# Kernel tuning notes

Measured on AMD Instinct MI355X. Metric: run time of the kernel, lower is better.

## Reference

```python
import jax, jax.numpy as jnp
import numpy as np
from jax import lax

BIT_SIZE = 8
ES_SIZE = 1


def posit_quantize(x, nbits=BIT_SIZE, es=ES_SIZE):
    """Round x to the nearest posit(nbits, es) representable value (round-to-nearest
    of the fraction given the regime/exponent-dependent fraction width)."""
    sign = jnp.sign(x)
    a = jnp.abs(x)
    safe = jnp.where(a > 0, a, jnp.ones_like(a))
    logx = jnp.floor(jnp.log2(safe))            # binade exponent
    ipow = 2 ** es                               # 2^es, python int
    k = jnp.floor(logx / ipow)                   # regime value
    regime_len = jnp.where(k >= 0, k + 2, -k + 1)
    fbits = jnp.clip(nbits - 1 - regime_len - es, 0, 23)  # fraction bits left
    scale = jnp.exp2(logx)
    frac = safe / scale                          # in [1, 2)
    step = jnp.exp2(fbits)
    q = jnp.round(frac * step) / step * scale
    maxpos = jnp.float32(2.0 ** ((nbits - 2) * ipow))
    minpos = jnp.float32(2.0 ** (-(nbits - 2) * ipow))
    q = jnp.clip(q, minpos, maxpos)
    return jnp.where(a > 0, sign * q, jnp.zeros_like(x))


def pq(x):
    # straight-through quantizer (forward value is exact posit rounding)
    return x + lax.stop_gradient(posit_quantize(x) - x)


def conv2d(x, w):  # NCHW, OIHW, valid, stride 1
    return lax.conv_general_dilated(x, w, (1, 1), 'VALID',
                                    dimension_numbers=('NCHW', 'OIHW', 'NCHW'))


def maxpool2(x):
    return lax.reduce_window(x, -jnp.inf, lax.max,
                             (1, 1, 2, 2), (1, 1, 2, 2), 'VALID')


def setup_inputs() -> dict:
    key = jax.random.key(0)
    ks = jax.random.split(key, 9)
    B = 4096
    x = jax.random.normal(ks[0], (B, 1, 28, 28), jnp.float32)
    def init_w(k, shape, fan_in):
        bound = 1.0 / np.sqrt(fan_in)
        return jax.random.uniform(k, shape, jnp.float32, -bound, bound)
    conv1_w = init_w(ks[1], (32, 1, 3, 3), 1 * 9)
    conv1_b = init_w(ks[2], (32,), 1 * 9)
    conv2_w = init_w(ks[3], (64, 32, 3, 3), 32 * 9)
    conv2_b = init_w(ks[4], (64,), 32 * 9)
    fc1_w = init_w(ks[5], (128, 12 * 12 * 64), 12 * 12 * 64)
    fc1_b = init_w(ks[6], (128,), 12 * 12 * 64)
    fc2_w = init_w(ks[7], (10, 128), 128)
    fc2_b = init_w(ks[8], (10,), 128)
    return dict(x=x, conv1_w=conv1_w, conv1_b=conv1_b, conv2_w=conv2_w,
                conv2_b=conv2_b, fc1_w=fc1_w, fc1_b=fc1_b,
                fc2_w=fc2_w, fc2_b=fc2_b)


def reference(x, conv1_w, conv1_b, conv2_w, conv2_b, fc1_w, fc1_b, fc2_w, fc2_b):
    # PositizedConv2d: posit-quantize activations and weights, conv in fp32, add bias
    h = conv2d(pq(x), pq(conv1_w)) + conv1_b[None, :, None, None]   # [B,32,26,26]
    h = jax.nn.relu(h)
    h = conv2d(pq(h), pq(conv2_w)) + conv2_b[None, :, None, None]   # [B,64,24,24]
    h = jax.nn.relu(h)
    h = maxpool2(h)                                                  # [B,64,12,12]
    # dropout layers are identity in eval mode
    h = h.reshape(-1, 12 * 12 * 64)
    h = jax.nn.relu(jnp.dot(pq(h), pq(fc1_w).T) + fc1_b)             # [B,128]
    out = jnp.dot(pq(h), pq(fc2_w).T) + fc2_b                        # [B,10]
    return out
```

## Files before the change

kernel.cpp:

```cpp
#include <hip/hip_runtime.h>

using u16 = unsigned short;
using u32 = unsigned int;
typedef __attribute__((ext_vector_type(8))) short bf16x8;
typedef __attribute__((ext_vector_type(4))) float f32x4;

__device__ __forceinline__ float posit_q(float x) {
    float a = __builtin_fabsf(x);
    u32 u = __float_as_uint(a);
    int logx = (int)(u >> 23) - 127;
    logx = logx < -60 ? -60 : (logx > 60 ? 60 : logx);
    float frac = __uint_as_float((u & 0x007fffffu) | 0x3f800000u);
    int k = logx >> 1;
    int rl = (k >= 0) ? (k + 2) : (1 - k);
    int fb = 6 - rl; fb = fb < 0 ? 0 : fb;
    float step = (float)(1 << fb);
    float q = rintf(frac * step) * __uint_as_float((u32)(127 + logx - fb) << 23);
    q = fminf(fmaxf(q, 0x1p-12f), 0x1p12f);
    return (a > 0.0f) ? copysignf(q, x) : 0.0f;
}

__device__ __forceinline__ float b2f(u16 v) { return __uint_as_float((u32)v << 16); }
__device__ __forceinline__ u16 f2b(float f) { return (u16)(__float_as_uint(f) >> 16); }

__device__ __forceinline__ void lut_init(int tid, float* lut) {
    if (tid < 256) {
        int e = tid - 127;
        float m = 0.f;
        if (e >= -12 && e <= 12) {
            int k = e >> 1;
            int rl = max(k + 2, 1 - k);
            int fb = max(6 - rl, 0);
            m = __uint_as_float((u32)(150 + e - fb) << 23) * 1.5f;
        }
        lut[tid] = m;
    }
}
__device__ __forceinline__ u32 pq_pos_raw(float x, const float* __restrict__ lut) {
    u32 u = __float_as_uint(x);
    float c = lut[u >> 23];
    float q = (x + c) - c;
    q = fminf(fmaxf(q, 0x1p-12f), 0x1p12f);
    return u == 0u ? 0u : __float_as_uint(q);
}

__global__ __launch_bounds__(256) void prep_kernel(
    const float* __restrict__ w1, const float* __restrict__ w2,
    const float* __restrict__ fw2,
    float* __restrict__ w1q, u16* __restrict__ w2frag, float* __restrict__ fc2wq) {
    int i = blockIdx.x * 256 + threadIdx.x;
    if (i < 288)  w1q[i]   = posit_q(w1[i]);
    if (i < 1280) fc2wq[i] = posit_q(fw2[i]);
    if (i < 18432) {
        int e = i & 7, lane = (i >> 3) & 63, c9 = i >> 9;
        int kc = c9 % 9, nt = c9 / 9;
        int n = nt * 16 + (lane & 15);
        int ci = ((lane >> 4) << 3) + e;
        w2frag[i] = f2b(posit_q(w2[n * 288 + ci * 9 + kc]));
    }
}

__global__ __launch_bounds__(256) void prep2_kernel(
    const float* __restrict__ fw1, u16* __restrict__ fc1wqF) {
    int i = blockIdx.x * 256 + threadIdx.x;
    int e = i & 7, lane = (i >> 3) & 63, c = i >> 9;
    int kk = c % 288, nt = c / 288;
    int n = nt * 16 + (lane & 15);
    int k = kk * 32 + ((lane >> 4) << 3) + e;
    fc1wqF[i] = f2b(posit_q(fw1[(size_t)n * 9216 + k]));
}

#define PLS 5416
__global__ __launch_bounds__(512, 4) void conv_fused_kernel(
    const float* __restrict__ x, const float* __restrict__ w1q, const float* __restrict__ b1,
    const u16* __restrict__ w2frag, const float* __restrict__ b2,
    const float* __restrict__ fw1, u16* __restrict__ fc1wq, u16* __restrict__ pooled) {
    __shared__ __align__(16) float sX[784];
    __shared__ __align__(16) u16 sH1[4 * PLS];
    __shared__ __align__(16) u16 sPool[64 * 152];
    __shared__ float sLut[256];
    int img = blockIdx.x, tid = threadIdx.x;
    int wave = tid >> 6, lane = tid & 63;
    int col = lane & 15, quad = lane >> 4;

    lut_init(tid, sLut);

    for (int i = tid; i < 784; i += 512) sX[i] = posit_q(x[(size_t)img * 784 + i]);
    if (tid < 288) fc1wq[(size_t)img * 288 + tid] = f2b(posit_q(fw1[(size_t)img * 288 + tid]));

    int ocp = tid & 15;
    float wreg[18];
#pragma unroll
    for (int j = 0; j < 18; ++j) wreg[j] = w1q[ocp * 18 + j];
    float bias0 = b1[ocp * 2], bias1 = b1[ocp * 2 + 1];

    __syncthreads();

    int pgrp = tid >> 4;
    u16* h1dst = &sH1[(ocp >> 2) * PLS + 2 * (ocp & 3)];
    for (int it = 0; it < 22; ++it) {
        int p = it * 32 + pgrp;
        if (p < 676) {
            int y = p / 26, xx = p - y * 26;
            const float* px = &sX[y * 28 + xx];
            float in9[9];
#pragma unroll
            for (int r = 0; r < 3; ++r)
#pragma unroll
                for (int c = 0; c < 3; ++c) in9[r * 3 + c] = px[r * 28 + c];
            float a0 = bias0, a1 = bias1;
#pragma unroll
            for (int j = 0; j < 9; ++j) {
                a0 = fmaf(wreg[j], in9[j], a0);
                a1 = fmaf(wreg[9 + j], in9[j], a1);
            }
            u32 r0 = pq_pos_raw(fmaxf(a0, 0.f), sLut);
            u32 r1 = pq_pos_raw(fmaxf(a1, 0.f), sLut);
            *(u32*)&h1dst[p * 8] = (r0 >> 16) | (r1 & 0xFFFF0000u);
        }
    }

    __syncthreads();
    int npair = wave & 1, mq = wave >> 1;
    bf16x8 bfrag[2][9];
#pragma unroll
    for (int j = 0; j < 2; ++j)
#pragma unroll
        for (int kc = 0; kc < 9; ++kc)
            bfrag[j][kc] = *(const bf16x8*)(w2frag + (((npair * 2 + j) * 9 + kc) * 64 + lane) * 8);
    float cb0 = b2[(npair * 2) * 16 + col];
    float cb1 = b2[(npair * 2 + 1) * 16 + col];
    int poolb0 = ((npair * 2) * 16 + col) * 152;
    int poolb1 = ((npair * 2 + 1) * 16 + col) * 152;
    const u16* aplane = &sH1[quad * PLS];

    for (int t = 0; t < 9; ++t) {
        int mt = mq * 9 + t;
        int m = mt * 16 + col;
        int pp = m >> 2, wi = m & 3;
        int py = pp / 12, px_ = pp - py * 12;
        int oh = 2 * py + (wi >> 1), ow = 2 * px_ + (wi & 1);
        const u16* ap = aplane + (oh * 26 + ow) * 8;
        f32x4 acc0 = {0.f, 0.f, 0.f, 0.f}, acc1 = {0.f, 0.f, 0.f, 0.f};
#pragma unroll
        for (int kc = 0; kc < 9; ++kc) {
            int kh = kc / 3, kw = kc - kh * 3;
            bf16x8 af = *(const bf16x8*)(ap + (kh * 26 + kw) * 8);
            acc0 = __builtin_amdgcn_mfma_f32_16x16x32_bf16(af, bfrag[0][kc], acc0, 0, 0, 0);
            acc1 = __builtin_amdgcn_mfma_f32_16x16x32_bf16(af, bfrag[1][kc], acc1, 0, 0, 0);
        }
        float mx0 = fmaxf(fmaxf(acc0[0], acc0[1]), fmaxf(acc0[2], acc0[3]));
        float mx1 = fmaxf(fmaxf(acc1[0], acc1[1]), fmaxf(acc1[2], acc1[3]));
        sPool[poolb0 + mt * 4 + quad] = (u16)(pq_pos_raw(fmaxf(mx0 + cb0, 0.f), sLut) >> 16);
        sPool[poolb1 + mt * 4 + quad] = (u16)(pq_pos_raw(fmaxf(mx1 + cb1, 0.f), sLut) >> 16);
    }
    __syncthreads();

    for (int u = tid; u < 1152; u += 512) {
        int c = u / 18, g = u - c * 18;
        uint4 v = *(const uint4*)&sPool[c * 152 + g * 8];
        *(uint4*)(pooled + (size_t)img * 9216 + c * 144 + g * 8) = v;
    }
}

#define AS 2328
__global__ __launch_bounds__(512, 4) void fc1_part_kernel(const u16* __restrict__ pooled,
    const u16* __restrict__ fc1wqF, float* __restrict__ part) {
    __shared__ __align__(16) char smem[16 * AS * 2];
    u16* sA = (u16*)smem;
    float* sAcc = (float*)smem;
    int blk = blockIdx.x, tid = threadIdx.x;
    int mb = blk >> 2, ks = blk & 3;
    int wave = tid >> 6, lane = tid & 63;
    int row = lane & 15, quad = lane >> 4;

    {
        const u16* src = pooled + (size_t)mb * 16 * 9216 + ks * 2304;
        for (int i = tid; i < 4608; i += 512) {
            int r = i / 288, o = i - r * 288;
            *(uint4*)&sA[r * AS + o * 8] = *(const uint4*)(src + (size_t)r * 9216 + o * 8);
        }
    }
    __syncthreads();

    const bf16x8* bbase = (const bf16x8*)fc1wqF + (size_t)(ks * 72 + wave * 9) * 64 + lane;
    const u16* abase = &sA[row * AS + wave * 288 + quad * 8];
    f32x4 acc[8];
#pragma unroll
    for (int nt = 0; nt < 8; ++nt) acc[nt] = f32x4{0.f, 0.f, 0.f, 0.f};
#pragma unroll 1
    for (int k2 = 0; k2 < 9; ++k2) {
        bf16x8 a = *(const bf16x8*)(abase + k2 * 32);
        bf16x8 b[8];
#pragma unroll
        for (int nt = 0; nt < 8; ++nt)
            b[nt] = bbase[((size_t)nt * 288 + k2) * 64];
#pragma unroll
        for (int nt = 0; nt < 8; ++nt)
            acc[nt] = __builtin_amdgcn_mfma_f32_16x16x32_bf16(a, b[nt], acc[nt], 0, 0, 0);
    }
    __syncthreads();
    if (wave < 4) {
#pragma unroll
        for (int nt = 0; nt < 8; ++nt)
#pragma unroll
            for (int r = 0; r < 4; ++r)
                sAcc[wave * 2112 + (quad * 4 + r) * 132 + nt * 16 + row] = acc[nt][r];
    }
    __syncthreads();
    if (wave >= 4) {
#pragma unroll
        for (int nt = 0; nt < 8; ++nt)
#pragma unroll
            for (int r = 0; r < 4; ++r)
                sAcc[(wave - 4) * 2112 + (quad * 4 + r) * 132 + nt * 16 + row] += acc[nt][r];
    }
    __syncthreads();
    for (int e = tid; e < 2048; e += 512) {
        int o = (e >> 7) * 132 + (e & 127);
        part[(size_t)blk * 2048 + e] = sAcc[o] + sAcc[2112 + o] + sAcc[4224 + o] + sAcc[6336 + o];
    }
}

__global__ __launch_bounds__(256) void fc2_red_kernel(const float* __restrict__ part,
    const float* __restrict__ fc1b, const float* __restrict__ fc2wq,
    const float* __restrict__ fc2b, float* __restrict__ out) {
    __shared__ __align__(16) u16 sFc1[2048];
    __shared__ float sW2[1280];
    __shared__ float sB2[16];
    __shared__ float sLut[256];
    int mb = blockIdx.x, tid = threadIdx.x;
    lut_init(tid, sLut);
    for (int i = tid; i < 1280; i += 256) sW2[i] = fc2wq[i];
    if (tid < 10) sB2[tid] = fc2b[tid];
    __syncthreads();
    const float* pb = part + (size_t)mb * 4 * 2048;
    for (int e = tid; e < 2048; e += 256) {
        float s = pb[e] + pb[2048 + e] + pb[4096 + e] + pb[6144 + e];
        sFc1[e] = (u16)(pq_pos_raw(fmaxf(s + fc1b[e & 127], 0.f), sLut) >> 16);
    }
    __syncthreads();
    if (tid < 160) {
        int il = tid / 10, oc = tid - il * 10;
        float s = sB2[oc];
        const u16* hp = &sFc1[il * 128];
        const float* wp = &sW2[oc * 128];
#pragma unroll
        for (int k = 0; k < 128; ++k) s = fmaf(b2f(hp[k]), wp[k], s);
        out[(size_t)(mb * 16 + il) * 10 + oc] = s;
    }
}

extern "C" void kernel_launch(void* const* d_in, const int* in_sizes, int n_in,
                              void* d_out, int out_size, void* d_ws, size_t ws_size,
                              hipStream_t stream) {
    const float* x    = (const float*)d_in[0];
    const float* w1   = (const float*)d_in[1];
    const float* b1   = (const float*)d_in[2];
    const float* w2   = (const float*)d_in[3];
    const float* b2   = (const float*)d_in[4];
    const float* fw1  = (const float*)d_in[5];
    const float* fb1  = (const float*)d_in[6];
    const float* fw2  = (const float*)d_in[7];
    const float* fb2  = (const float*)d_in[8];
    float* out = (float*)d_out;

    char* ws = (char*)d_ws;
    float* w1q     = (float*)(ws + 0);
    float* fc2wq   = (float*)(ws + 1280);
    u16*   w2frag  = (u16*)(ws + 6400);
    u16*   fc1wqF  = (u16*)(ws + 43520);
    u16*   fc1dmy  = (u16*)(ws + 2402816);
    u16*   pooled  = (u16*)(ws + 4762112);
    float* part    = (float*)(ws + 80259584);

    prep_kernel<<<72, 256, 0, stream>>>(w1, w2, fw2, w1q, w2frag, fc2wq);
    prep2_kernel<<<4608, 256, 0, stream>>>(fw1, fc1wqF);
    conv_fused_kernel<<<4096, 512, 0, stream>>>(x, w1q, b1, w2frag, b2, fw1, fc1dmy, pooled);
    fc1_part_kernel<<<1024, 512, 0, stream>>>(pooled, fc1wqF, part);
    fc2_red_kernel<<<256, 256, 0, stream>>>(part, fb1, fc2wq, fb2, out);
}
```

Measured before the change: 249.6 us.

## Restructure conv2 MFMA loop: one N-tile per wave, 18 M-tile accumulators

Each wave now owns a single 16-column output-channel tile and half of the M tiles, keeping 18 accumulators live across a kc-outer loop. Instead of preloading 18 B fragments into registers, it loads one B fragment per kc and reuses it across the 18 M tiles. This lowers register pressure from the B fragments and raises the number of independent MFMAs in flight, but each A fragment from LDS is now read once per N tile rather than shared across two, which adds LDS traffic. The 72 accumulator VGPRs may also affect occupancy.

```diff
diff --git a/kernel.cpp b/kernel.cpp
--- a/kernel.cpp
+++ b/kernel.cpp
@@ -121,38 +121,40 @@
     }
 
     __syncthreads();
-    int npair = wave & 1, mq = wave >> 1;
-    bf16x8 bfrag[2][9];
-#pragma unroll
-    for (int j = 0; j < 2; ++j)
-#pragma unroll
-        for (int kc = 0; kc < 9; ++kc)
-            bfrag[j][kc] = *(const bf16x8*)(w2frag + (((npair * 2 + j) * 9 + kc) * 64 + lane) * 8);
-    float cb0 = b2[(npair * 2) * 16 + col];
-    float cb1 = b2[(npair * 2 + 1) * 16 + col];
-    int poolb0 = ((npair * 2) * 16 + col) * 152;
-    int poolb1 = ((npair * 2 + 1) * 16 + col) * 152;
+    int nt = wave & 3, mhalf = wave >> 2;
+    float cb = b2[nt * 16 + col];
+    int poolb = (nt * 16 + col) * 152;
     const u16* aplane = &sH1[quad * PLS];
 
-    for (int t = 0; t < 9; ++t) {
-        int mt = mq * 9 + t;
+    int aoff[18];
+#pragma unroll
+    for (int t = 0; t < 18; ++t) {
+        int mt = mhalf * 18 + t;
         int m = mt * 16 + col;
         int pp = m >> 2, wi = m & 3;
         int py = pp / 12, px_ = pp - py * 12;
         int oh = 2 * py + (wi >> 1), ow = 2 * px_ + (wi & 1);
-        const u16* ap = aplane + (oh * 26 + ow) * 8;
-        f32x4 acc0 = {0.f, 0.f, 0.f, 0.f}, acc1 = {0.f, 0.f, 0.f, 0.f};
-#pragma unroll
-        for (int kc = 0; kc < 9; ++kc) {
-            int kh = kc / 3, kw = kc - kh * 3;
-            bf16x8 af = *(const bf16x8*)(ap + (kh * 26 + kw) * 8);
-            acc0 = __builtin_amdgcn_mfma_f32_16x16x32_bf16(af, bfrag[0][kc], acc0, 0, 0, 0);
-            acc1 = __builtin_amdgcn_mfma_f32_16x16x32_bf16(af, bfrag[1][kc], acc1, 0, 0, 0);
-        }
-        float mx0 = fmaxf(fmaxf(acc0[0], acc0[1]), fmaxf(acc0[2], acc0[3]));
-        float mx1 = fmaxf(fmaxf(acc1[0], acc1[1]), fmaxf(acc1[2], acc1[3]));
-        sPool[poolb0 + mt * 4 + quad] = (u16)(pq_pos_raw(fmaxf(mx0 + cb0, 0.f), sLut) >> 16);
-        sPool[poolb1 + mt * 4 + quad] = (u16)(pq_pos_raw(fmaxf(mx1 + cb1, 0.f), sLut) >> 16);
+        aoff[t] = (oh * 26 + ow) * 8;
+    }
+    f32x4 acc[18];
+#pragma unroll
+    for (int t = 0; t < 18; ++t) acc[t] = f32x4{0.f, 0.f, 0.f, 0.f};
+#pragma unroll 1
+    for (int kc = 0; kc < 9; ++kc) {
+        int kh = kc / 3, kw = kc - kh * 3;
+        bf16x8 bfr = *(const bf16x8*)(w2frag + ((nt * 9 + kc) * 64 + lane) * 8);
+        int delta = (kh * 26 + kw) * 8;
+#pragma unroll
+        for (int t = 0; t < 18; ++t) {
+            bf16x8 af = *(const bf16x8*)(aplane + aoff[t] + delta);
+            acc[t] = __builtin_amdgcn_mfma_f32_16x16x32_bf16(af, bfr, acc[t], 0, 0, 0);
+        }
+    }
+#pragma unroll
+    for (int t = 0; t < 18; ++t) {
+        int mt = mhalf * 18 + t;
+        float mx = fmaxf(fmaxf(acc[t][0], acc[t][1]), fmaxf(acc[t][2], acc[t][3]));
+        sPool[poolb + mt * 4 + quad] = (u16)(pq_pos_raw(fmaxf(mx + cb, 0.f), sLut) >> 16);
     }
     __syncthreads();
 
```

After: 293.0 us. 17.4% more time.

## Merge prep kernels and fuse fc2 reduction into fc1 via last-block election

Applied to the files above, without the earlier changes.

The two weight-prep kernels become one launch that also zeroes a per-row-block counter array. The separate fc2 reduction kernel is folded into fc1_part_kernel: each block atomically bumps its row block's counter, and the fourth (last) block to arrive sums the partials and computes fc2 in place. This removes two kernel launches and the gaps between them, at the cost of atomics, thread fences and a serialized tail in the electing block.

```diff
diff --git a/kernel.cpp b/kernel.cpp
--- a/kernel.cpp
+++ b/kernel.cpp
@@ -44,30 +44,32 @@
     return u == 0u ? 0u : __float_as_uint(q);
 }
 
-__global__ __launch_bounds__(256) void prep_kernel(
+__global__ __launch_bounds__(256) void prep_all_kernel(
     const float* __restrict__ w1, const float* __restrict__ w2,
-    const float* __restrict__ fw2,
-    float* __restrict__ w1q, u16* __restrict__ w2frag, float* __restrict__ fc2wq) {
-    int i = blockIdx.x * 256 + threadIdx.x;
-    if (i < 288)  w1q[i]   = posit_q(w1[i]);
-    if (i < 1280) fc2wq[i] = posit_q(fw2[i]);
-    if (i < 18432) {
-        int e = i & 7, lane = (i >> 3) & 63, c9 = i >> 9;
-        int kc = c9 % 9, nt = c9 / 9;
+    const float* __restrict__ fw2, const float* __restrict__ fw1,
+    float* __restrict__ w1q, u16* __restrict__ w2frag, float* __restrict__ fc2wq,
+    u16* __restrict__ fc1wqF, int* __restrict__ cnt) {
+    int b = blockIdx.x;
+    if (b < 4608) {
+        int i = b * 256 + threadIdx.x;
+        int e = i & 7, lane = (i >> 3) & 63, c = i >> 9;
+        int kk = c % 288, nt = c / 288;
         int n = nt * 16 + (lane & 15);
-        int ci = ((lane >> 4) << 3) + e;
-        w2frag[i] = f2b(posit_q(w2[n * 288 + ci * 9 + kc]));
-    }
-}
-
-__global__ __launch_bounds__(256) void prep2_kernel(
-    const float* __restrict__ fw1, u16* __restrict__ fc1wqF) {
-    int i = blockIdx.x * 256 + threadIdx.x;
-    int e = i & 7, lane = (i >> 3) & 63, c = i >> 9;
-    int kk = c % 288, nt = c / 288;
-    int n = nt * 16 + (lane & 15);
-    int k = kk * 32 + ((lane >> 4) << 3) + e;
-    fc1wqF[i] = f2b(posit_q(fw1[(size_t)n * 9216 + k]));
+        int k = kk * 32 + ((lane >> 4) << 3) + e;
+        fc1wqF[i] = f2b(posit_q(fw1[(size_t)n * 9216 + k]));
+    } else {
+        int i = (b - 4608) * 256 + threadIdx.x;
+        if (i < 256)  cnt[i] = 0;
+        if (i < 288)  w1q[i]   = posit_q(w1[i]);
+        if (i < 1280) fc2wq[i] = posit_q(fw2[i]);
+        {
+            int e = i & 7, lane = (i >> 3) & 63, c9 = i >> 9;
+            int kc = c9 % 9, nt = c9 / 9;
+            int n = nt * 16 + (lane & 15);
+            int ci = ((lane >> 4) << 3) + e;
+            w2frag[i] = f2b(posit_q(w2[n * 288 + ci * 9 + kc]));
+        }
+    }
 }
 
 #define PLS 5416
@@ -165,8 +167,11 @@
 
 #define AS 2328
 __global__ __launch_bounds__(512, 4) void fc1_part_kernel(const u16* __restrict__ pooled,
-    const u16* __restrict__ fc1wqF, float* __restrict__ part) {
+    const u16* __restrict__ fc1wqF, float* __restrict__ part, int* __restrict__ cnt,
+    const float* __restrict__ fc1b, const float* __restrict__ fc2wq,
+    const float* __restrict__ fc2b, float* __restrict__ out) {
     __shared__ __align__(16) char smem[16 * AS * 2];
+    __shared__ int sElect;
     u16* sA = (u16*)smem;
     float* sAcc = (float*)smem;
     int blk = blockIdx.x, tid = threadIdx.x;
@@ -220,24 +225,24 @@
         int o = (e >> 7) * 132 + (e & 127);
         part[(size_t)blk * 2048 + e] = sAcc[o] + sAcc[2112 + o] + sAcc[4224 + o] + sAcc[6336 + o];
     }
-}
-
-__global__ __launch_bounds__(256) void fc2_red_kernel(const float* __restrict__ part,
-    const float* __restrict__ fc1b, const float* __restrict__ fc2wq,
-    const float* __restrict__ fc2b, float* __restrict__ out) {
-    __shared__ __align__(16) u16 sFc1[2048];
-    __shared__ float sW2[1280];
-    __shared__ float sB2[16];
-    __shared__ float sLut[256];
-    int mb = blockIdx.x, tid = threadIdx.x;
-    lut_init(tid, sLut);
-    for (int i = tid; i < 1280; i += 256) sW2[i] = fc2wq[i];
+
+    __threadfence();
+    if (tid == 0) sElect = (atomicAdd(&cnt[mb], 1) == 3);
+    __syncthreads();
+    if (!sElect) return;
+    __threadfence();
+    u16*   sFc1  = (u16*)smem;
+    float* sW2   = (float*)(smem + 4096);
+    float* sB2   = (float*)(smem + 9216);
+    float* sLut2 = (float*)(smem + 9280);
+    lut_init(tid, sLut2);
+    for (int i = tid; i < 1280; i += 512) sW2[i] = fc2wq[i];
     if (tid < 10) sB2[tid] = fc2b[tid];
     __syncthreads();
     const float* pb = part + (size_t)mb * 4 * 2048;
-    for (int e = tid; e < 2048; e += 256) {
+    for (int e = tid; e < 2048; e += 512) {
         float s = pb[e] + pb[2048 + e] + pb[4096 + e] + pb[6144 + e];
-        sFc1[e] = (u16)(pq_pos_raw(fmaxf(s + fc1b[e & 127], 0.f), sLut) >> 16);
+        sFc1[e] = (u16)(pq_pos_raw(fmaxf(s + fc1b[e & 127], 0.f), sLut2) >> 16);
     }
     __syncthreads();
     if (tid < 160) {
@@ -273,10 +278,9 @@
     u16*   fc1dmy  = (u16*)(ws + 2402816);
     u16*   pooled  = (u16*)(ws + 4762112);
     float* part    = (float*)(ws + 80259584);
-
-    prep_kernel<<<72, 256, 0, stream>>>(w1, w2, fw2, w1q, w2frag, fc2wq);
-    prep2_kernel<<<4608, 256, 0, stream>>>(fw1, fc1wqF);
+    int*   cnt     = (int*)(ws + 88648192);
+
+    prep_all_kernel<<<4680, 256, 0, stream>>>(w1, w2, fw2, fw1, w1q, w2frag, fc2wq, fc1wqF, cnt);
     conv_fused_kernel<<<4096, 512, 0, stream>>>(x, w1q, b1, w2frag, b2, fw1, fc1dmy, pooled);
-    fc1_part_kernel<<<1024, 512, 0, stream>>>(pooled, fc1wqF, part);
-    fc2_red_kernel<<<256, 256, 0, stream>>>(part, fb1, fc2wq, fb2, out);
-}
+    fc1_part_kernel<<<1024, 512, 0, stream>>>(pooled, fc1wqF, part, cnt, fb1, fc2wq, fb2, out);
+}
```

Result: slower. 518.7 us (+107.8%).
